# Kernel optimization log

Hardware: AMD Instinct MI355X
Metric: run time of the kernel (lower is better)

The kernel has to match this reference:

```python
import jax, jax.numpy as jnp
import numpy as np

OUT_FEATURES = 4096
IN_FEATURES = 4096
GROUP_SIZE = 128


def setup_inputs() -> dict:
    key = jax.random.key(0)
    k1, k2, k3, k4, k5 = jax.random.split(key, 5)
    x = jax.random.normal(k1, (4, 2048, IN_FEATURES), dtype=jnp.float32)
    # two 4-bit codes per byte-like int32 element
    packed = jax.random.randint(k2, (OUT_FEATURES * IN_FEATURES // 2,), 0, 256, dtype=jnp.int32)
    n_groups = OUT_FEATURES * IN_FEATURES // GROUP_SIZE
    scales = jax.random.uniform(k3, (n_groups,), dtype=jnp.float32) * 0.02 + 1e-3
    offsets = jax.random.normal(k4, (n_groups,), dtype=jnp.float32) * 0.01
    bias = jax.random.normal(k5, (OUT_FEATURES,), dtype=jnp.float32)
    return {"x": x, "packed": packed, "scales": scales, "offsets": offsets, "bias": bias}


def _dequant(packed, scales, offsets):
    # unpack low/high nibbles -> int codes in [0, 15]
    low = packed & 0xF
    high = (packed >> 4) & 0xF
    codes = jnp.stack([low, high], axis=-1).reshape(-1).astype(jnp.float32)  # [out*in]
    # per-group affine dequant: w = code * scale + offset
    w = codes.reshape(-1, GROUP_SIZE) * scales[:, None] + offsets[:, None]
    return w.reshape(OUT_FEATURES, IN_FEATURES)


def reference(x, packed, scales, offsets, bias):
    weight = _dequant(packed, scales, offsets)  # [out, in]
    # F.linear: x @ W^T + b
    return jnp.einsum('bsi,oi->bso', x, weight) + bias
```

## Files before the change

### kernel.cpp

```cpp
#include <hip/hip_runtime.h>
#include <stdint.h>

#define IN_F   4096
#define OUT_F  4096
#define M_TOT  8192
#define BK     32
#define NT     (IN_F / BK)
#define BUF_B  32768
#define NBUF   4

typedef __bf16 bf16x8 __attribute__((ext_vector_type(8)));
typedef float  floatx4 __attribute__((ext_vector_type(4)));

#define WAITVM(N) asm volatile("s_waitcnt vmcnt(" #N ")" ::: "memory")
#define FENCE_BARRIER() do {                          \
    asm volatile("" ::: "memory");                    \
    __builtin_amdgcn_s_barrier();                     \
    asm volatile("" ::: "memory");                    \
    __builtin_amdgcn_sched_barrier(0);                \
} while (0)

__device__ __forceinline__ unsigned short f2bf_bits(float f) {
    union { float f; uint32_t u; } v; v.f = f;
    uint32_t r = v.u + 0x7FFF + ((v.u >> 16) & 1);
    return (unsigned short)(r >> 16);
}

__device__ __forceinline__ void gl_lds16(const void* g, void* l) {
    __builtin_amdgcn_global_load_lds(
        (const __attribute__((address_space(1))) void*)g,
        (__attribute__((address_space(3))) void*)l, 16, 0, 0);
}

__global__ void cvt_x_kernel(const float* __restrict__ x, ushort* __restrict__ xb) {
    int i = blockIdx.x * blockDim.x + threadIdx.x;
    const float4* xp = reinterpret_cast<const float4*>(x);
    float4 a = xp[2 * i], b = xp[2 * i + 1];
    uint4 o;
    o.x = (uint32_t)f2bf_bits(a.x) | ((uint32_t)f2bf_bits(a.y) << 16);
    o.y = (uint32_t)f2bf_bits(a.z) | ((uint32_t)f2bf_bits(a.w) << 16);
    o.z = (uint32_t)f2bf_bits(b.x) | ((uint32_t)f2bf_bits(b.y) << 16);
    o.w = (uint32_t)f2bf_bits(b.z) | ((uint32_t)f2bf_bits(b.w) << 16);
    reinterpret_cast<uint4*>(xb)[i] = o;
}

__global__ void dequant_kernel(const int* __restrict__ packed,
                               const float* __restrict__ scales,
                               const float* __restrict__ offsets,
                               ushort* __restrict__ wb) {
    int i = blockIdx.x * blockDim.x + threadIdx.x;
    int4 p = reinterpret_cast<const int4*>(packed)[i];
    int g = i >> 4;
    float s = scales[g], off = offsets[g];
    uint4 ov;
    {
        int pv = p.x;
        unsigned w0 = f2bf_bits((float)(pv & 0xF) * s + off);
        unsigned w1 = f2bf_bits((float)((pv >> 4) & 0xF) * s + off);
        ov.x = w0 | (w1 << 16);
    }
    {
        int pv = p.y;
        unsigned w0 = f2bf_bits((float)(pv & 0xF) * s + off);
        unsigned w1 = f2bf_bits((float)((pv >> 4) & 0xF) * s + off);
        ov.y = w0 | (w1 << 16);
    }
    {
        int pv = p.z;
        unsigned w0 = f2bf_bits((float)(pv & 0xF) * s + off);
        unsigned w1 = f2bf_bits((float)((pv >> 4) & 0xF) * s + off);
        ov.z = w0 | (w1 << 16);
    }
    {
        int pv = p.w;
        unsigned w0 = f2bf_bits((float)(pv & 0xF) * s + off);
        unsigned w1 = f2bf_bits((float)((pv >> 4) & 0xF) * s + off);
        ov.w = w0 | (w1 << 16);
    }
    reinterpret_cast<uint4*>(wb)[i] = ov;
}

__launch_bounds__(512, 2)
__global__ void gemm_kernel(const ushort* __restrict__ A,
                            const ushort* __restrict__ B,
                            const float* __restrict__ bias,
                            float* __restrict__ C) {
    __shared__ __align__(16) char smem[NBUF * BUF_B];

    const int tid  = threadIdx.x;
    const int wave = tid >> 6;
    const int lane = tid & 63;
    const int quad = lane >> 4;
    const int l16  = lane & 15;
    const int wm   = wave >> 2;
    const int wn   = wave & 3;

    int id = blockIdx.y * gridDim.x + blockIdx.x;
    id = (id & 7) * 64 + (id >> 3);
    const int bn = id & 15;
    const int bm = id >> 4;

    const int c0 = tid, c1 = 512 + tid;
    const int r0 = c0 >> 2, r1 = c1 >> 2;
    const int cb0 = ((c0 & 3) << 4) ^ (((r0 >> 1) & 3) << 4);
    const int cb1 = ((c1 & 3) << 4) ^ (((r1 >> 1) & 3) << 4);
    const ushort* gA0 = A + (size_t)(bm * 256 + r0) * IN_F + (cb0 >> 1);
    const ushort* gA1 = A + (size_t)(bm * 256 + r1) * IN_F + (cb1 >> 1);
    const ushort* gB0 = B + (size_t)(bn * 256 + r0) * IN_F + (cb0 >> 1);
    const ushort* gB1 = B + (size_t)(bn * 256 + r1) * IN_F + (cb1 >> 1);
    const int ldsA0 = wave * 1024;
    const int ldsA1 = 8192 + wave * 1024;
    const int ldsB0 = 16384 + wave * 1024;
    const int ldsB1 = 24576 + wave * 1024;

    auto STAGE = [&](int t) {
        char* base = smem + (t & (NBUF - 1)) * BUF_B;
        const int ko = t * BK;
        gl_lds16(gA0 + ko, base + ldsA0);
        gl_lds16(gA1 + ko, base + ldsA1);
        gl_lds16(gB0 + ko, base + ldsB0);
        gl_lds16(gB1 + ko, base + ldsB1);
    };

    const int arowb = wm * 128 + l16;
    const int browb = wn * 64 + l16;
    const int aswz = ((arowb >> 1) & 3) << 4;
    const int bswz = ((browb >> 1) & 3) << 4;
    const int acol = (((quad * 16) ^ aswz) >> 1);
    const int bcol = (((quad * 16) ^ bswz) >> 1);

    floatx4 acc[8][4] = {};
    bf16x8 afA[8], bfA[4], afB[8], bfB[4];

    auto READ = [&](bf16x8* af, bf16x8* bfr, int t) {
        const ushort* bufp = (const ushort*)(smem + (t & (NBUF - 1)) * BUF_B);
#pragma unroll
        for (int mi = 0; mi < 8; ++mi)
            af[mi] = *reinterpret_cast<const bf16x8*>(bufp + (arowb + mi * 16) * 32 + acol);
#pragma unroll
        for (int ni = 0; ni < 4; ++ni)
            bfr[ni] = *reinterpret_cast<const bf16x8*>(bufp + 8192 + (browb + ni * 16) * 32 + bcol);
    };

    auto MFMA32 = [&](const bf16x8* af, const bf16x8* bfr) {
        __builtin_amdgcn_s_setprio(1);
#pragma unroll
        for (int mi = 0; mi < 8; ++mi)
#pragma unroll
            for (int ni = 0; ni < 4; ++ni)
                acc[mi][ni] = __builtin_amdgcn_mfma_f32_16x16x32_bf16(
                    af[mi], bfr[ni], acc[mi][ni], 0, 0, 0);
        __builtin_amdgcn_s_setprio(0);
    };

    STAGE(0); STAGE(1); STAGE(2);
    WAITVM(4);
    FENCE_BARRIER();
    READ(afA, bfA, 0);

#pragma unroll 1
    for (int t = 0; t < NT; t += 2) {
        if (t + 3 < NT) STAGE(t + 3);
        if (t + 1 < NT) READ(afB, bfB, t + 1);
        MFMA32(afA, bfA);
        WAITVM(4);
        FENCE_BARRIER();
        if (t + 4 < NT) STAGE(t + 4);
        if (t + 2 < NT) READ(afA, bfA, t + 2);
        MFMA32(afB, bfB);
        WAITVM(4);
        FENCE_BARRIER();
    }

    const int ccol = bn * 256 + wn * 64 + l16;
    const float* bp = bias + ccol;
    float* Cp = C + (size_t)(bm * 256 + wm * 128 + quad * 4) * OUT_F + ccol;
#pragma unroll
    for (int mi = 0; mi < 8; ++mi) {
#pragma unroll
        for (int ni = 0; ni < 4; ++ni) {
            float bv = bp[ni * 16];
#pragma unroll
            for (int r = 0; r < 4; ++r)
                Cp[(size_t)(mi * 16 + r) * OUT_F + ni * 16] = acc[mi][ni][r] + bv;
        }
    }
}

extern "C" void kernel_launch(void* const* d_in, const int* in_sizes, int n_in,
                              void* d_out, int out_size, void* d_ws, size_t ws_size,
                              hipStream_t stream) {
    const float* x       = (const float*)d_in[0];
    const int*   packed  = (const int*)d_in[1];
    const float* scales  = (const float*)d_in[2];
    const float* offsets = (const float*)d_in[3];
    const float* bias    = (const float*)d_in[4];
    float* out = (float*)d_out;

    ushort* xb = (ushort*)d_ws;
    ushort* wb = (ushort*)((char*)d_ws + (size_t)M_TOT * IN_F * 2);

    cvt_x_kernel<<<16384, 256, 0, stream>>>(x, xb);
    dequant_kernel<<<8192, 256, 0, stream>>>(packed, scales, offsets, wb);

    dim3 grid(OUT_F / 256, M_TOT / 256);
    gemm_kernel<<<grid, 512, 0, stream>>>(xb, wb, bias, out);
}
```

Baseline: 487.6 us.

## Restructure GEMM main loop into half-tile phases with barriers around MFMA

Replaces the register double-buffered loop (two full fragment sets, 32 MFMAs per phase) with a per-tile schedule split into two half-M phases. Each phase reads a quarter of the fragments, issues half of the next tile's global-to-LDS loads, then hits a barrier and an lgkmcnt wait before 16 MFMAs. This lowers register pressure and interleaves load issue across waves in a ping-pong style. In exchange it adds two to three barriers per K step and removes the overlap of LDS reads with MFMA inside a wave.

Result: no change. 493.0 us (+1.1%).

```diff
diff --git a/kernel.cpp b/kernel.cpp
--- a/kernel.cpp
+++ b/kernel.cpp
@@ -13,6 +13,10 @@
 typedef float  floatx4 __attribute__((ext_vector_type(4)));
 
 #define WAITVM(N) asm volatile("s_waitcnt vmcnt(" #N ")" ::: "memory")
+#define LGKM0() do {                                   \
+    asm volatile("s_waitcnt lgkmcnt(0)" ::: "memory"); \
+    __builtin_amdgcn_sched_barrier(0);                 \
+} while (0)
 #define FENCE_BARRIER() do {                          \
     asm volatile("" ::: "memory");                    \
     __builtin_amdgcn_s_barrier();                     \
@@ -113,7 +117,7 @@
     const int ldsB0 = 16384 + wave * 1024;
     const int ldsB1 = 24576 + wave * 1024;
 
-    auto STAGE = [&](int t) {
+    auto STAGE_FULL = [&](int t) {
         char* base = smem + (t & (NBUF - 1)) * BUF_B;
         const int ko = t * BK;
         gl_lds16(gA0 + ko, base + ldsA0);
@@ -121,6 +125,18 @@
         gl_lds16(gB0 + ko, base + ldsB0);
         gl_lds16(gB1 + ko, base + ldsB1);
     };
+    auto STAGE_A = [&](int t) {
+        char* base = smem + (t & (NBUF - 1)) * BUF_B;
+        const int ko = t * BK;
+        gl_lds16(gA0 + ko, base + ldsA0);
+        gl_lds16(gA1 + ko, base + ldsA1);
+    };
+    auto STAGE_B = [&](int t) {
+        char* base = smem + (t & (NBUF - 1)) * BUF_B;
+        const int ko = t * BK;
+        gl_lds16(gB0 + ko, base + ldsB0);
+        gl_lds16(gB1 + ko, base + ldsB1);
+    };
 
     const int arowb = wm * 128 + l16;
     const int browb = wn * 64 + l16;
@@ -130,47 +146,73 @@
     const int bcol = (((quad * 16) ^ bswz) >> 1);
 
     floatx4 acc[8][4] = {};
-    bf16x8 afA[8], bfA[4], afB[8], bfB[4];
-
-    auto READ = [&](bf16x8* af, bf16x8* bfr, int t) {
-        const ushort* bufp = (const ushort*)(smem + (t & (NBUF - 1)) * BUF_B);
-#pragma unroll
-        for (int mi = 0; mi < 8; ++mi)
-            af[mi] = *reinterpret_cast<const bf16x8*>(bufp + (arowb + mi * 16) * 32 + acol);
+    bf16x8 a4[4], b4[4];
+
+    auto READ_A = [&](const ushort* bufp, int mh) {
+#pragma unroll
+        for (int mi = 0; mi < 4; ++mi)
+            a4[mi] = *reinterpret_cast<const bf16x8*>(
+                bufp + (arowb + (mh * 4 + mi) * 16) * 32 + acol);
+    };
+    auto READ_B = [&](const ushort* bufp) {
 #pragma unroll
         for (int ni = 0; ni < 4; ++ni)
-            bfr[ni] = *reinterpret_cast<const bf16x8*>(bufp + 8192 + (browb + ni * 16) * 32 + bcol);
-    };
-
-    auto MFMA32 = [&](const bf16x8* af, const bf16x8* bfr) {
-        __builtin_amdgcn_s_setprio(1);
-#pragma unroll
-        for (int mi = 0; mi < 8; ++mi)
-#pragma unroll
-            for (int ni = 0; ni < 4; ++ni)
-                acc[mi][ni] = __builtin_amdgcn_mfma_f32_16x16x32_bf16(
-                    af[mi], bfr[ni], acc[mi][ni], 0, 0, 0);
-        __builtin_amdgcn_s_setprio(0);
-    };
-
-    STAGE(0); STAGE(1); STAGE(2);
+            b4[ni] = *reinterpret_cast<const bf16x8*>(
+                bufp + 8192 + (browb + ni * 16) * 32 + bcol);
+    };
+
+#define MFMA16(MH) do {                                              \
+    __builtin_amdgcn_s_setprio(1);                                   \
+    _Pragma("unroll")                                                \
+    for (int mi = 0; mi < 4; ++mi)                                   \
+        _Pragma("unroll")                                            \
+        for (int ni = 0; ni < 4; ++ni)                               \
+            acc[(MH) * 4 + mi][ni] =                                 \
+                __builtin_amdgcn_mfma_f32_16x16x32_bf16(             \
+                    a4[mi], b4[ni], acc[(MH) * 4 + mi][ni], 0, 0, 0);\
+    __builtin_amdgcn_s_setprio(0);                                   \
+} while (0)
+
+    STAGE_FULL(0); STAGE_FULL(1); STAGE_FULL(2);
     WAITVM(4);
     FENCE_BARRIER();
-    READ(afA, bfA, 0);
 
 #pragma unroll 1
-    for (int t = 0; t < NT; t += 2) {
-        if (t + 3 < NT) STAGE(t + 3);
-        if (t + 1 < NT) READ(afB, bfB, t + 1);
-        MFMA32(afA, bfA);
+    for (int t = 0; t < NT - 3; ++t) {
+        const ushort* bufp = (const ushort*)(smem + (t & (NBUF - 1)) * BUF_B);
+        READ_A(bufp, 0);
+        READ_B(bufp);
+        STAGE_A(t + 3);
+        FENCE_BARRIER();
+        LGKM0();
+        MFMA16(0);
+        FENCE_BARRIER();
+        READ_A(bufp, 1);
+        STAGE_B(t + 3);
         WAITVM(4);
         FENCE_BARRIER();
-        if (t + 4 < NT) STAGE(t + 4);
-        if (t + 2 < NT) READ(afA, bfA, t + 2);
-        MFMA32(afB, bfB);
-        WAITVM(4);
-        FENCE_BARRIER();
-    }
+        LGKM0();
+        MFMA16(1);
+        FENCE_BARRIER();
+    }
+
+    {
+        const ushort* bufp = (const ushort*)(smem + ((NT - 3) & (NBUF - 1)) * BUF_B);
+        READ_A(bufp, 0); READ_B(bufp);
+        FENCE_BARRIER(); LGKM0(); MFMA16(0); FENCE_BARRIER();
+        READ_A(bufp, 1);
+        WAITVM(0);
+        FENCE_BARRIER(); LGKM0(); MFMA16(1); FENCE_BARRIER();
+    }
+#pragma unroll
+    for (int t = NT - 2; t < NT; ++t) {
+        const ushort* bufp = (const ushort*)(smem + (t & (NBUF - 1)) * BUF_B);
+        READ_A(bufp, 0); READ_B(bufp);
+        MFMA16(0);
+        READ_A(bufp, 1);
+        MFMA16(1);
+    }
+#undef MFMA16
 
     const int ccol = bn * 256 + wn * 64 + l16;
     const float* bp = bias + ccol;
```
